# Optimization experiments

Hardware: AMD Instinct MI355X
Metric: run time of the kernel (lower is better)

The kernel has to match this reference:

```python
import jax, jax.numpy as jnp
import numpy as np
import math

IN_C = 512
OUT_C = 512
K = 3
STYLE = 512
EPS = 1e-8
MOD_SCALE = 1.0 / math.sqrt(STYLE)        # EqualLinear scale (lr_mul=1)
CONV_SCALE = 1.0 / math.sqrt(IN_C * K * K)  # ModulatedConv2d scale


def setup_inputs() -> dict:
    key = jax.random.key(0)
    k1, k2, k3, k4 = jax.random.split(key, 4)
    return {
        "x": jax.random.normal(k1, (8, IN_C, 64, 64), dtype=jnp.float32),
        "style": jax.random.normal(k2, (8, STYLE), dtype=jnp.float32),
        "mod_weight": jax.random.normal(k3, (IN_C, STYLE), dtype=jnp.float32),
        "mod_bias": jnp.ones((IN_C,), dtype=jnp.float32),
        "weight": jax.random.normal(k4, (1, OUT_C, IN_C, K, K), dtype=jnp.float32),
    }


def _per_sample_conv(xi, wi):
    # xi: [in_c, H, W], wi: [out_c, in_c, K, K]
    out = jax.lax.conv_general_dilated(
        xi[None], wi, window_strides=(1, 1), padding="SAME",
        dimension_numbers=("NCHW", "OIHW", "NCHW"))
    return out[0]


def reference(x, style, mod_weight, mod_bias, weight):
    # EqualLinear modulation: s = style @ (W*scale)^T + bias  -> [B, in_c]
    s = style @ (mod_weight * MOD_SCALE).T + mod_bias
    # per-sample modulated weight: [B, out_c, in_c, K, K]
    w = CONV_SCALE * weight * s[:, None, :, None, None]
    demod = jax.lax.rsqrt(jnp.sum(w * w, axis=(2, 3, 4), keepdims=True) + EPS)
    w = w * demod
    # grouped conv (groups=batch) == vmap of per-sample conv
    out = jax.vmap(_per_sample_conv)(x, w)  # [B, out_c, H, W]
    return out
```

## Files before the change

### kernel.cpp

```cpp
#include <hip/hip_runtime.h>
#include <hip/hip_bf16.h>

typedef __attribute__((ext_vector_type(8))) short bf16x8;
typedef __attribute__((ext_vector_type(16))) float f32x16;
typedef unsigned int u32;

#define MOD_SCALE 0.04419417382415922f
#define CONV_SCALE 0.014731391274719742f

__device__ __forceinline__ unsigned short f2bf(float f) {
  union { float f; u32 u; } v; v.f = f;
  u32 r = v.u + 0x7fffu + ((v.u >> 16) & 1u);
  return (unsigned short)(r >> 16);
}

__device__ __forceinline__ void gload_lds16(const void* g, void* l) {
  __builtin_amdgcn_global_load_lds(
      (const __attribute__((address_space(1))) u32*)g,
      (__attribute__((address_space(3))) u32*)l, 16, 0, 0);
}

__device__ __forceinline__ int swz(int c) { return c ^ ((c >> 3) & 1); }

__global__ void k_prep(const float* __restrict__ wsrc, ushort* __restrict__ wb,
                       float* __restrict__ wsq, float* __restrict__ zerobuf,
                       const float* __restrict__ style, const float* __restrict__ mw,
                       const float* __restrict__ mb, float* __restrict__ s) {
  if (blockIdx.x < 1024) {
    int idx = blockIdx.x * 256 + threadIdx.x;
    int oc = idx >> 9, ic = idx & 511;
    int icb = ic >> 4, icr = ic & 15;
    if (blockIdx.x == 0 && threadIdx.x < 16) zerobuf[threadIdx.x] = 0.f;
    const float* wp = wsrc + (size_t)idx * 9;
    float sq = 0.f;
    #pragma unroll
    for (int tap = 0; tap < 9; ++tap) {
      float v = wp[tap];
      sq += v * v;
      wb[((tap * 32 + icb) * 512 + oc) * 16 + icr] = f2bf(v);
    }
    wsq[idx] = sq;
  } else {
    int idx = (blockIdx.x - 1024) * 256 + threadIdx.x;
    int b = idx >> 9, ic = idx & 511;
    const float4* wr = (const float4*)(mw + ic * 512);
    const float4* sr = (const float4*)(style + b * 512);
    float acc = 0.f;
    #pragma unroll 4
    for (int k = 0; k < 128; ++k) {
      float4 a = wr[k], c = sr[k];
      acc += a.x * c.x + a.y * c.y + a.z * c.z + a.w * c.w;
    }
    s[idx] = acc * MOD_SCALE + mb[ic];
  }
}

__global__ void k_xform(const float* __restrict__ x, const float* __restrict__ s,
                        ushort* __restrict__ xsb) {
  const int y = blockIdx.x, b = blockIdx.y;
  const int t = threadIdx.x;
  const int px = t & 63, icq = t >> 6;
  #pragma unroll
  for (int i = 0; i < 8; ++i) {
    int icb = i * 4 + icq;
    union { ushort u[16]; uint4 v[2]; } pk;
    #pragma unroll
    for (int j = 0; j < 16; ++j) {
      int ic = icb * 16 + j;
      float v = x[(b * 512 + ic) * 4096 + y * 64 + px] * s[b * 512 + ic];
      pk.u[j] = f2bf(v);
    }
    ushort* dst = xsb + ((size_t)((b * 64 + y) * 32 + icb) * 64 + px) * 16;
    *(uint4*)dst = pk.v[0];
    *(uint4*)(dst + 8) = pk.v[1];
  }
}

#define ABYTES 18432
#define BBYTES 21120
#define BUFB   39552
__global__ __launch_bounds__(256, 2) void k_conv(
    const ushort* __restrict__ wb, const ushort* __restrict__ xsb,
    const float* __restrict__ wsq, const float* __restrict__ s,
    const float* __restrict__ zerobuf, float* __restrict__ out) {
  const int yb = blockIdx.x, ocb = blockIdx.y, b = blockIdx.z;
  const int t = threadIdx.x;
  const int wv = t >> 6, l = t & 63;
  const int lc = l & 31, lh = l >> 5;
  const int y0 = yb * 8, oc0 = ocb * 64;

  extern __shared__ char smem[];
  float* red = (float*)(smem + 2 * BUFB);
  float* dss = (float*)(smem + 2 * BUFB + 1024);

  f32x16 acc[2][2][2];
  #pragma unroll
  for (int rr = 0; rr < 2; ++rr)
    #pragma unroll
    for (int ocf = 0; ocf < 2; ++ocf)
      #pragma unroll
      for (int pxf = 0; pxf < 2; ++pxf)
        #pragma unroll
        for (int k = 0; k < 16; ++k)
          acc[rr][ocf][pxf][k] = 0.f;

  const char* asrc[5];
  #pragma unroll
  for (int i = 0; i < 5; ++i) {
    int cid = i * 256 + t;
    int tap = cid >> 7, pc = cid & 127;
    int c = swz(pc);
    int oc_l = c >> 1, h = c & 1;
    asrc[i] = (const char*)wb + (size_t)tap * 524288 + (oc0 + oc_l) * 32 + h * 16;
  }
  const char* bsrc[6];
  int bstride[6];
  #pragma unroll
  for (int i = 0; i < 6; ++i) {
    int cid = i * 256 + t;
    int pr = cid / 132, prem = cid - pr * 132;
    int lrem = swz(prem);
    int yy = y0 - 1 + pr;
    bool interior = (lrem >= 2) && (lrem < 130) && ((unsigned)yy < 64u);
    bsrc[i] = interior
        ? (const char*)xsb + (size_t)(b * 64 + yy) * 65536 + (lrem - 2) * 16
        : (const char*)zerobuf;
    bstride[i] = interior ? 2048 : 0;
  }

  int aswzo; { int c = lc * 2 + lh; aswzo = swz(c) * 16; }
  int bswzo[3][2];
  #pragma unroll
  for (int dx = 0; dx < 3; ++dx)
    #pragma unroll
    for (int pxf = 0; pxf < 2; ++pxf) {
      int c = (pxf * 32 + dx + lc) * 2 + lh;
      bswzo[dx][pxf] = swz(c) * 16;
    }

  auto STAGE = [&](int bo, int icb) {
    char* Ab = smem + bo;
    char* Bb = Ab + ABYTES;
    const int aoff = icb * 16384;
    #pragma unroll
    for (int i = 0; i < 4; ++i)
      gload_lds16(asrc[i] + aoff, Ab + i * 4096 + wv * 1024);
    if (t < 128)
      gload_lds16(asrc[4] + aoff, Ab + 16384 + wv * 1024);
    #pragma unroll
    for (int i = 0; i < 5; ++i)
      gload_lds16(bsrc[i] + icb * bstride[i], Bb + i * 4096 + wv * 1024);
    if (t < 40)
      gload_lds16(bsrc[5] + icb * bstride[5], Bb + 20480);
  };

  auto COMPUTE = [&](int bo) {
    const char* Ab = smem + bo;
    const char* Bb = Ab + ABYTES;
    #pragma unroll
    for (int dx = 0; dx < 3; ++dx) {
      bf16x8 bfr[4][2];
      #pragma unroll
      for (int j = 0; j < 4; ++j)
        #pragma unroll
        for (int pxf = 0; pxf < 2; ++pxf)
          bfr[j][pxf] = *(const bf16x8*)(Bb + (wv * 2 + j) * 2112 + bswzo[dx][pxf]);
      #pragma unroll
      for (int dy = 0; dy < 3; ++dy) {
        const int tap = dy * 3 + dx;
        bf16x8 af[2];
        #pragma unroll
        for (int ocf = 0; ocf < 2; ++ocf)
          af[ocf] = *(const bf16x8*)(Ab + tap * 2048 + ocf * 1024 + aswzo);
        #pragma unroll
        for (int rr = 0; rr < 2; ++rr)
          #pragma unroll
          for (int ocf = 0; ocf < 2; ++ocf)
            #pragma unroll
            for (int pxf = 0; pxf < 2; ++pxf)
              acc[rr][ocf][pxf] = __builtin_amdgcn_mfma_f32_32x32x16_bf16(
                  af[ocf], bfr[rr + dy][pxf], acc[rr][ocf][pxf], 0, 0, 0);
      }
    }
  };

  STAGE(0, 0);

  {
    const int oc_l = t & 63, kq = t >> 6;
    const float4* wq = (const float4*)(wsq + (oc0 + oc_l) * 512) + kq * 32;
    const float4* sp = (const float4*)(s + b * 512) + kq * 32;
    float part = 0.f;
    #pragma unroll 4
    for (int k = 0; k < 32; ++k) {
      float4 a = wq[k], c = sp[k];
      part += a.x * c.x * c.x + a.y * c.y * c.y + a.z * c.z * c.z + a.w * c.w * c.w;
    }
    red[t] = part;
  }
  __syncthreads();
  if (t < 64)
    dss[t] = CONV_SCALE * rsqrtf(
        CONV_SCALE * CONV_SCALE * (red[t] + red[t + 64] + red[t + 128] + red[t + 192]) + 1e-8f);

  #pragma unroll 1
  for (int it = 0; it < 32; it += 2) {
    STAGE(BUFB, it + 1);
    COMPUTE(0);
    __syncthreads();
    if (it < 30) STAGE(0, it + 2);
    COMPUTE(BUFB);
    __syncthreads();
  }

  #pragma unroll
  for (int rr = 0; rr < 2; ++rr) {
    const int y_row = y0 + wv * 2 + rr;
    #pragma unroll
    for (int ocf = 0; ocf < 2; ++ocf) {
      #pragma unroll
      for (int pxf = 0; pxf < 2; ++pxf) {
        #pragma unroll
        for (int reg = 0; reg < 16; ++reg) {
          int oc_l = ocf * 32 + (reg & 3) + 8 * (reg >> 2) + 4 * lh;
          out[(size_t)(b * 512 + oc0 + oc_l) * 4096 + y_row * 64 + pxf * 32 + lc]
              = acc[rr][ocf][pxf][reg] * dss[oc_l];
        }
      }
    }
  }
}

extern "C" void kernel_launch(void* const* d_in, const int* in_sizes, int n_in,
                              void* d_out, int out_size, void* d_ws, size_t ws_size,
                              hipStream_t stream) {
  const float* x     = (const float*)d_in[0];
  const float* style = (const float*)d_in[1];
  const float* mw    = (const float*)d_in[2];
  const float* mb    = (const float*)d_in[3];
  const float* wsrc  = (const float*)d_in[4];
  float* out = (float*)d_out;

  char* ws = (char*)d_ws;
  float*  zerobuf = (float*)(ws + 0);
  float*  s       = (float*)(ws + 256);
  float*  wsq     = (float*)(ws + 33024);
  ushort* wb      = (ushort*)(ws + 1081600);
  ushort* xsb     = (ushort*)(ws + 5800192);

  hipFuncSetAttribute(reinterpret_cast<const void*>(k_conv),
                      hipFuncAttributeMaxDynamicSharedMemorySize, 2 * BUFB + 1280);

  k_prep<<<dim3(1040), dim3(256), 0, stream>>>(wsrc, wb, wsq, zerobuf, style, mw, mb, s);
  k_xform<<<dim3(64, 8), dim3(256), 0, stream>>>(x, s, xsb);
  k_conv<<<dim3(8, 8, 8), dim3(256), 2 * BUFB + 1280, stream>>>(wb, xsb, wsq, s, zerobuf, out);
}
```

Measured before the change: 172.7 us.

## Restructure conv LDS staging with deeper prefetch, fine-grained waits and padded halo

Rewrites the conv kernel's global-to-LDS staging into a uniform 10-load scheme. Horizontal halo padding is handled by a zeroed LDS column instead of swizzled zero loads, and the XOR swizzle is dropped. Both buffers are prefetched up front, and __syncthreads is replaced with explicit vmcnt waits and barriers so loads for the next stage stay in flight while computing. It also raises MFMA wave priority around the compute burst and stages the weight tile through LDS in k_prep for coalesced reads. Without the swizzle, LDS bank conflicts may return.

After: 191.6 us. +11.0%, slower.

```diff
diff --git a/kernel.cpp b/kernel.cpp
--- a/kernel.cpp
+++ b/kernel.cpp
@@ -20,28 +20,33 @@
       (__attribute__((address_space(3))) u32*)l, 16, 0, 0);
 }
 
-__device__ __forceinline__ int swz(int c) { return c ^ ((c >> 3) & 1); }
-
 __global__ void k_prep(const float* __restrict__ wsrc, ushort* __restrict__ wb,
                        float* __restrict__ wsq, float* __restrict__ zerobuf,
                        const float* __restrict__ style, const float* __restrict__ mw,
                        const float* __restrict__ mb, float* __restrict__ s) {
+  __shared__ float wtile[2304];
+  const int t = threadIdx.x;
   if (blockIdx.x < 1024) {
-    int idx = blockIdx.x * 256 + threadIdx.x;
+    const float4* s4 = (const float4*)(wsrc + (size_t)blockIdx.x * 2304);
+    float4* w4 = (float4*)wtile;
+    w4[t] = s4[t];
+    w4[t + 256] = s4[t + 256];
+    if (t < 64) w4[t + 512] = s4[t + 512];
+    __syncthreads();
+    int idx = blockIdx.x * 256 + t;
     int oc = idx >> 9, ic = idx & 511;
     int icb = ic >> 4, icr = ic & 15;
-    if (blockIdx.x == 0 && threadIdx.x < 16) zerobuf[threadIdx.x] = 0.f;
-    const float* wp = wsrc + (size_t)idx * 9;
+    if (blockIdx.x == 0 && t < 16) zerobuf[t] = 0.f;
     float sq = 0.f;
     #pragma unroll
     for (int tap = 0; tap < 9; ++tap) {
-      float v = wp[tap];
+      float v = wtile[t * 9 + tap];
       sq += v * v;
       wb[((tap * 32 + icb) * 512 + oc) * 16 + icr] = f2bf(v);
     }
     wsq[idx] = sq;
   } else {
-    int idx = (blockIdx.x - 1024) * 256 + threadIdx.x;
+    int idx = (blockIdx.x - 1024) * 256 + t;
     int b = idx >> 9, ic = idx & 511;
     const float4* wr = (const float4*)(mw + ic * 512);
     const float4* sr = (const float4*)(style + b * 512);
@@ -77,8 +82,13 @@
 }
 
 #define ABYTES 18432
-#define BBYTES 21120
-#define BUFB   39552
+#define BROW   2080
+#define BUFB   (ABYTES + 10 * BROW)
+#define TRASHO (2 * BUFB)
+#define REDOFF (2 * BUFB + 1024)
+#define DSSOFF (2 * BUFB + 2048)
+#define SMEMSZ (2 * BUFB + 2048 + 256)
+
 __global__ __launch_bounds__(256, 2) void k_conv(
     const ushort* __restrict__ wb, const ushort* __restrict__ xsb,
     const float* __restrict__ wsq, const float* __restrict__ s,
@@ -90,8 +100,8 @@
   const int y0 = yb * 8, oc0 = ocb * 64;
 
   extern __shared__ char smem[];
-  float* red = (float*)(smem + 2 * BUFB);
-  float* dss = (float*)(smem + 2 * BUFB + 1024);
+  float* red = (float*)(smem + REDOFF);
+  float* dss = (float*)(smem + DSSOFF);
 
   f32x16 acc[2][2][2];
   #pragma unroll
@@ -104,59 +114,57 @@
         for (int k = 0; k < 16; ++k)
           acc[rr][ocf][pxf][k] = 0.f;
 
-  const char* asrc[5];
-  #pragma unroll
-  for (int i = 0; i < 5; ++i) {
-    int cid = i * 256 + t;
-    int tap = cid >> 7, pc = cid & 127;
-    int c = swz(pc);
-    int oc_l = c >> 1, h = c & 1;
-    asrc[i] = (const char*)wb + (size_t)tap * 524288 + (oc0 + oc_l) * 32 + h * 16;
-  }
-  const char* bsrc[6];
-  int bstride[6];
-  #pragma unroll
-  for (int i = 0; i < 6; ++i) {
-    int cid = i * 256 + t;
-    int pr = cid / 132, prem = cid - pr * 132;
-    int lrem = swz(prem);
-    int yy = y0 - 1 + pr;
-    bool interior = (lrem >= 2) && (lrem < 130) && ((unsigned)yy < 64u);
-    bsrc[i] = interior
-        ? (const char*)xsb + (size_t)(b * 64 + yy) * 65536 + (lrem - 2) * 16
-        : (const char*)zerobuf;
-    bstride[i] = interior ? 2048 : 0;
-  }
-
-  int aswzo; { int c = lc * 2 + lh; aswzo = swz(c) * 16; }
-  int bswzo[3][2];
+  const char* gsrc[10];
+  int gstr[10];
+  #pragma unroll
+  for (int i = 0; i < 10; ++i) {
+    int s0 = i * 256 + t;
+    if (s0 < 1152) {
+      int tap = s0 >> 7, cc = s0 & 127, oc_l = cc >> 1, h = cc & 1;
+      gsrc[i] = (const char*)wb + (size_t)tap * 524288 + (size_t)(oc0 + oc_l) * 32 + h * 16;
+      gstr[i] = 16384;
+    } else if (s0 < 2432) {
+      int c = s0 - 1152, r = c >> 7, cc = c & 127, px = cc >> 1, h = cc & 1;
+      int yy = y0 - 1 + r;
+      bool ok = (unsigned)yy < 64u;
+      gsrc[i] = ok ? (const char*)xsb + ((size_t)(b * 64 + yy) * 2048 + px) * 32 + h * 16
+                   : (const char*)zerobuf;
+      gstr[i] = ok ? 2048 : 0;
+    } else {
+      gsrc[i] = (const char*)zerobuf;
+      gstr[i] = 0;
+    }
+  }
+
+  int apo[2];
+  apo[0] = (lc * 2 + lh) * 16;
+  apo[1] = apo[0] + 1024;
+  int boff[3][2];
   #pragma unroll
   for (int dx = 0; dx < 3; ++dx)
     #pragma unroll
     for (int pxf = 0; pxf < 2; ++pxf) {
-      int c = (pxf * 32 + dx + lc) * 2 + lh;
-      bswzo[dx][pxf] = swz(c) * 16;
+      int px = pxf * 32 + dx - 1 + lc;
+      boff[dx][pxf] = ((unsigned)px < 64u) ? px * 32 + lh * 16 : 2048 + lh * 16;
     }
 
   auto STAGE = [&](int bo, int icb) {
-    char* Ab = smem + bo;
-    char* Bb = Ab + ABYTES;
-    const int aoff = icb * 16384;
-    #pragma unroll
-    for (int i = 0; i < 4; ++i)
-      gload_lds16(asrc[i] + aoff, Ab + i * 4096 + wv * 1024);
-    if (t < 128)
-      gload_lds16(asrc[4] + aoff, Ab + 16384 + wv * 1024);
-    #pragma unroll
-    for (int i = 0; i < 5; ++i)
-      gload_lds16(bsrc[i] + icb * bstride[i], Bb + i * 4096 + wv * 1024);
-    if (t < 40)
-      gload_lds16(bsrc[5] + icb * bstride[5], Bb + 20480);
+    #pragma unroll
+    for (int i = 0; i < 10; ++i) {
+      char* dst;
+      if (i <= 3)      dst = smem + bo + (i * 256 + wv * 64) * 16;
+      else if (i == 4) dst = (wv < 2) ? smem + bo + (1024 + wv * 64) * 16
+                                      : smem + bo + ABYTES + (wv - 2) * 1024;
+      else if (i <= 8) dst = smem + bo + ABYTES + ((i - 5) * 2 + 1 + (wv >> 1)) * BROW + (wv & 1) * 1024;
+      else             dst = (wv < 2) ? smem + bo + ABYTES + 9 * BROW + wv * 1024
+                                      : smem + TRASHO;
+      gload_lds16(gsrc[i] + (size_t)(icb * gstr[i]), dst);
+    }
   };
 
   auto COMPUTE = [&](int bo) {
     const char* Ab = smem + bo;
-    const char* Bb = Ab + ABYTES;
+    const char* Bb = smem + bo + ABYTES;
     #pragma unroll
     for (int dx = 0; dx < 3; ++dx) {
       bf16x8 bfr[4][2];
@@ -164,14 +172,16 @@
       for (int j = 0; j < 4; ++j)
         #pragma unroll
         for (int pxf = 0; pxf < 2; ++pxf)
-          bfr[j][pxf] = *(const bf16x8*)(Bb + (wv * 2 + j) * 2112 + bswzo[dx][pxf]);
-      #pragma unroll
-      for (int dy = 0; dy < 3; ++dy) {
-        const int tap = dy * 3 + dx;
-        bf16x8 af[2];
+          bfr[j][pxf] = *(const bf16x8*)(Bb + (wv * 2 + j) * BROW + boff[dx][pxf]);
+      bf16x8 af[3][2];
+      #pragma unroll
+      for (int dy = 0; dy < 3; ++dy)
         #pragma unroll
         for (int ocf = 0; ocf < 2; ++ocf)
-          af[ocf] = *(const bf16x8*)(Ab + tap * 2048 + ocf * 1024 + aswzo);
+          af[dy][ocf] = *(const bf16x8*)(Ab + (dy * 3 + dx) * 2048 + apo[ocf]);
+      __builtin_amdgcn_s_setprio(1);
+      #pragma unroll
+      for (int dy = 0; dy < 3; ++dy)
         #pragma unroll
         for (int rr = 0; rr < 2; ++rr)
           #pragma unroll
@@ -179,16 +189,19 @@
             #pragma unroll
             for (int pxf = 0; pxf < 2; ++pxf)
               acc[rr][ocf][pxf] = __builtin_amdgcn_mfma_f32_32x32x16_bf16(
-                  af[ocf], bfr[rr + dy][pxf], acc[rr][ocf][pxf], 0, 0, 0);
-      }
+                  af[dy][ocf], bfr[rr + dy][pxf], acc[rr][ocf][pxf], 0, 0, 0);
+      __builtin_amdgcn_s_setprio(0);
     }
   };
 
-  STAGE(0, 0);
-
+  if (t < 40) {
+    int q = t & 1, id = t >> 1;
+    int bi = id / 10, r = id - bi * 10;
+    *(uint4*)(smem + bi * BUFB + ABYTES + r * BROW + 2048 + q * 16) = uint4{0, 0, 0, 0};
+  }
   {
     const int oc_l = t & 63, kq = t >> 6;
-    const float4* wq = (const float4*)(wsq + (oc0 + oc_l) * 512) + kq * 32;
+    const float4* wq = (const float4*)(wsq + (size_t)(oc0 + oc_l) * 512) + kq * 32;
     const float4* sp = (const float4*)(s + b * 512) + kq * 32;
     float part = 0.f;
     #pragma unroll 4
@@ -198,19 +211,37 @@
     }
     red[t] = part;
   }
-  __syncthreads();
+  STAGE(0, 0);
+  STAGE(BUFB, 1);
+  asm volatile("s_waitcnt lgkmcnt(0)" ::: "memory");
+  asm volatile("s_barrier" ::: "memory");
   if (t < 64)
     dss[t] = CONV_SCALE * rsqrtf(
         CONV_SCALE * CONV_SCALE * (red[t] + red[t + 64] + red[t + 128] + red[t + 192]) + 1e-8f);
+  asm volatile("s_waitcnt vmcnt(10) lgkmcnt(0)" ::: "memory");
+  asm volatile("s_barrier" ::: "memory");
 
   #pragma unroll 1
   for (int it = 0; it < 32; it += 2) {
-    STAGE(BUFB, it + 1);
     COMPUTE(0);
-    __syncthreads();
-    if (it < 30) STAGE(0, it + 2);
+    asm volatile("s_barrier" ::: "memory");
+    if (it < 30) {
+      STAGE(0, it + 2);
+      asm volatile("s_waitcnt vmcnt(10)" ::: "memory");
+    } else {
+      asm volatile("s_waitcnt vmcnt(0)" ::: "memory");
+    }
+    asm volatile("s_barrier" ::: "memory");
+
     COMPUTE(BUFB);
-    __syncthreads();
+    asm volatile("s_barrier" ::: "memory");
+    if (it + 1 < 30) {
+      STAGE(BUFB, it + 3);
+      asm volatile("s_waitcnt vmcnt(10)" ::: "memory");
+    } else {
+      asm volatile("s_waitcnt vmcnt(0)" ::: "memory");
+    }
+    asm volatile("s_barrier" ::: "memory");
   }
 
   #pragma unroll
@@ -249,9 +280,9 @@
   ushort* xsb     = (ushort*)(ws + 5800192);
 
   hipFuncSetAttribute(reinterpret_cast<const void*>(k_conv),
-                      hipFuncAttributeMaxDynamicSharedMemorySize, 2 * BUFB + 1280);
+                      hipFuncAttributeMaxDynamicSharedMemorySize, SMEMSZ);
 
   k_prep<<<dim3(1040), dim3(256), 0, stream>>>(wsrc, wb, wsq, zerobuf, style, mw, mb, s);
   k_xform<<<dim3(64, 8), dim3(256), 0, stream>>>(x, s, xsb);
-  k_conv<<<dim3(8, 8, 8), dim3(256), 2 * BUFB + 1280, stream>>>(wb, xsb, wsq, s, zerobuf, out);
-}
+  k_conv<<<dim3(8, 8, 8), dim3(256), SMEMSZ, stream>>>(wb, xsb, wsq, s, zerobuf, out);
+}
```
